# Performance work log

Hardware: AMD Instinct MI355X
Metric: run time of the kernel (lower is better)

The kernel has to match this reference:

```python
import jax, jax.numpy as jnp
import numpy as np


def setup_inputs() -> dict:
    key = jax.random.key(0)
    k1, k2, k3, k4 = jax.random.split(key, 4)
    B, S, D = 8, 2048, 512
    scale = 1.0 / np.sqrt(D)
    return {
        "x": jax.random.normal(k1, (B, S, D), dtype=jnp.float32),
        "WQ": jax.random.normal(k2, (D, D), dtype=jnp.float32) * scale,
        "WK": jax.random.normal(k3, (D, D), dtype=jnp.float32) * scale,
        "WV": jax.random.normal(k4, (D, D), dtype=jnp.float32) * scale,
    }


def reference(x, WQ, WK, WV):
    # x: [B, S, D]; single-head scaled dot-product self-attention
    Q = jnp.einsum("bsd,de->bse", x, WQ)
    K = jnp.einsum("bsd,de->bse", x, WK)
    V = jnp.einsum("bsd,de->bse", x, WV)
    d_k = jnp.asarray(K.shape[-1], dtype=x.dtype)
    scores = jnp.einsum("bqd,bkd->bqk", Q, K) / jnp.sqrt(d_k)  # [B,S,S]
    weights = jax.nn.softmax(scores, axis=-1)
    return jnp.einsum("bqk,bkd->bqd", weights, V)
```

## Files before the change

kernel.cpp:

```cpp
#include <hip/hip_runtime.h>
#include <cstdint>
#include <cstddef>

#define B_ 8
#define S_ 2048
#define D_ 512

typedef float f32x4 __attribute__((ext_vector_type(4)));
typedef __bf16 bf16x8 __attribute__((ext_vector_type(8)));

__device__ __forceinline__ unsigned short f2bf(float f) {
    unsigned u = __builtin_bit_cast(unsigned, f);
    u += 0x7FFFu + ((u >> 16) & 1u);
    return (unsigned short)(u >> 16);
}

__device__ __forceinline__ void gld_lds16(const void* g, void* l) {
    __builtin_amdgcn_global_load_lds(
        (__attribute__((address_space(1))) void*)g,
        (__attribute__((address_space(3))) void*)l,
        16, 0, 0);
}

__global__ __launch_bounds__(256) void gemm_bt(
    const unsigned short* __restrict__ A,
    const unsigned short* __restrict__ B,
    void* __restrict__ Cv,
    int K, int lda, int ldb, int ldc,
    long long sA, long long sB, long long sC,
    float scale, int out_bf16, int ntn, int nbatch)
{
    __shared__ __align__(16) unsigned short lA[128 * 32];
    __shared__ __align__(16) unsigned short lB[128 * 32];

    const int lin = blockIdx.x;
    const int bz  = lin % nbatch;
    const int t   = lin / nbatch;
    const int tn  = t % ntn;
    const int tm  = t / ntn;

    A += (long long)bz * sA;
    B += (long long)bz * sB;
    const int m0 = tm * 128;
    const int n0 = tn * 128;
    const int tid  = threadIdx.x;
    const int lane = tid & 63;
    const int wave = tid >> 6;
    const int wm = (wave & 1) * 64;
    const int wn = (wave >> 1) * 64;

    f32x4 acc[4][4] = {};

    const int bo0 = wave * 2048;
    const int bo1 = bo0 + 1024;
    const int o0 = bo0 + lane * 16;
    const int o1 = bo1 + lane * 16;
    const int r0 = o0 >> 6, cp0 = (o0 & 63) >> 4;
    const int r1 = o1 >> 6, cp1 = (o1 & 63) >> 4;
    const int c0 = (cp0 ^ (r0 & 3)) << 3;
    const int c1 = (cp1 ^ (r1 & 3)) << 3;

    const unsigned short* A0 = A + (size_t)(m0 + r0) * lda + c0;
    const unsigned short* A1 = A + (size_t)(m0 + r1) * lda + c1;
    const unsigned short* B0 = B + (size_t)(n0 + r0) * ldb + c0;
    const unsigned short* B1 = B + (size_t)(n0 + r1) * ldb + c1;

    char* lAc = (char*)lA;
    char* lBc = (char*)lB;

    const int fr  = lane & 15;
    const int g   = lane >> 4;
    const int sx  = (g ^ (fr & 3)) << 3;

    for (int k0 = 0; k0 < K; k0 += 32) {
        __syncthreads();
        gld_lds16(A0 + k0, lAc + bo0);
        gld_lds16(A1 + k0, lAc + bo1);
        gld_lds16(B0 + k0, lBc + bo0);
        gld_lds16(B1 + k0, lBc + bo1);
        __syncthreads();

        bf16x8 af[4], bfr[4];
        #pragma unroll
        for (int tt = 0; tt < 4; ++tt) {
            af[tt]  = *(const bf16x8*)&lA[(wm + tt * 16 + fr) * 32 + sx];
            bfr[tt] = *(const bf16x8*)&lB[(wn + tt * 16 + fr) * 32 + sx];
        }
        #pragma unroll
        for (int mt = 0; mt < 4; ++mt)
            #pragma unroll
            for (int nt = 0; nt < 4; ++nt)
                acc[mt][nt] = __builtin_amdgcn_mfma_f32_16x16x32_bf16(
                    af[mt], bfr[nt], acc[mt][nt], 0, 0, 0);
    }

    const int col = lane & 15;
    const int rb  = (lane >> 4) * 4;
    if (out_bf16) {
        unsigned short* C = (unsigned short*)Cv + (long long)bz * sC;
        #pragma unroll
        for (int mt = 0; mt < 4; ++mt) {
            #pragma unroll
            for (int nt = 0; nt < 4; ++nt) {
                const int gc = n0 + wn + nt * 16 + col;
                #pragma unroll
                for (int r = 0; r < 4; ++r) {
                    const int gr = m0 + wm + mt * 16 + rb + r;
                    C[(size_t)gr * ldc + gc] = f2bf(acc[mt][nt][r] * scale);
                }
            }
        }
    } else {
        float* C = (float*)Cv + (long long)bz * sC;
        #pragma unroll
        for (int mt = 0; mt < 4; ++mt) {
            #pragma unroll
            for (int nt = 0; nt < 4; ++nt) {
                const int gc = n0 + wn + nt * 16 + col;
                #pragma unroll
                for (int r = 0; r < 4; ++r) {
                    const int gr = m0 + wm + mt * 16 + rb + r;
                    C[(size_t)gr * ldc + gc] = acc[mt][nt][r] * scale;
                }
            }
        }
    }
}

__global__ __launch_bounds__(256) void convert_x4(const float* __restrict__ x,
                                                  unsigned short* __restrict__ xb) {
    const size_t i = ((size_t)blockIdx.x * 256 + threadIdx.x) * 4;
    const float4 f = *(const float4*)(x + i);
    ushort4 u;
    u.x = f2bf(f.x); u.y = f2bf(f.y); u.z = f2bf(f.z); u.w = f2bf(f.w);
    *(ushort4*)(xb + i) = u;
}

__global__ __launch_bounds__(256) void convert_w(const float* __restrict__ WQ,
                                                 const float* __restrict__ WK,
                                                 const float* __restrict__ WV,
                                                 unsigned short* __restrict__ WT) {
    const int o = blockIdx.x * 256 + threadIdx.x;
    const float* W = blockIdx.y == 0 ? WQ : (blockIdx.y == 1 ? WK : WV);
    const int e = o >> 9, d = o & (D_ - 1);
    WT[(size_t)blockIdx.y * D_ * D_ + o] = f2bf(W[d * D_ + e]);
}

__global__ __launch_bounds__(256) void transpose_v(const unsigned short* __restrict__ V,
                                                   int ldv,
                                                   unsigned short* __restrict__ VT) {
    __shared__ unsigned short t[32][33];
    const int b  = blockIdx.z;
    const int s0 = blockIdx.x * 32;
    const int d0 = blockIdx.y * 32;
    const int tx = threadIdx.x & 31;
    const int ty = threadIdx.x >> 5;
    const unsigned short* Vb = V + (size_t)b * S_ * ldv;
    unsigned short* VTb = VT + (size_t)b * S_ * D_;
    #pragma unroll
    for (int j = 0; j < 32; j += 8)
        t[ty + j][tx] = Vb[(size_t)(s0 + ty + j) * ldv + d0 + tx];
    __syncthreads();
    #pragma unroll
    for (int j = 0; j < 32; j += 8)
        VTb[(size_t)(d0 + ty + j) * S_ + s0 + tx] = t[tx][ty + j];
}

__global__ __launch_bounds__(256) void softmax_rows(unsigned short* __restrict__ Smat) {
    const int tid = threadIdx.x;
    unsigned short* row = Smat + (size_t)blockIdx.x * S_;
    const uint4 raw = *(const uint4*)(row + tid * 8);
    const unsigned ru[4] = {raw.x, raw.y, raw.z, raw.w};
    float v[8];
    #pragma unroll
    for (int i = 0; i < 4; ++i) {
        v[2 * i]     = __builtin_bit_cast(float, (ru[i] & 0xFFFFu) << 16);
        v[2 * i + 1] = __builtin_bit_cast(float, ru[i] & 0xFFFF0000u);
    }
    float m = v[0];
    #pragma unroll
    for (int i = 1; i < 8; ++i) m = fmaxf(m, v[i]);
    #pragma unroll
    for (int off = 32; off > 0; off >>= 1) m = fmaxf(m, __shfl_xor(m, off, 64));
    __shared__ float red[4];
    const int wave = tid >> 6, lane = tid & 63;
    if (lane == 0) red[wave] = m;
    __syncthreads();
    m = fmaxf(fmaxf(red[0], red[1]), fmaxf(red[2], red[3]));

    float e[8], s = 0.f;
    #pragma unroll
    for (int i = 0; i < 8; ++i) { e[i] = __expf(v[i] - m); s += e[i]; }
    #pragma unroll
    for (int off = 32; off > 0; off >>= 1) s += __shfl_xor(s, off, 64);
    __syncthreads();
    if (lane == 0) red[wave] = s;
    __syncthreads();
    const float inv = 1.0f / (red[0] + red[1] + red[2] + red[3]);

    uint4 o;
    unsigned ov[4];
    #pragma unroll
    for (int i = 0; i < 4; ++i)
        ov[i] = (unsigned)f2bf(e[2 * i] * inv) |
                ((unsigned)f2bf(e[2 * i + 1] * inv) << 16);
    o.x = ov[0]; o.y = ov[1]; o.z = ov[2]; o.w = ov[3];
    *(uint4*)(row + tid * 8) = o;
}

extern "C" void kernel_launch(void* const* d_in, const int* in_sizes, int n_in,
                              void* d_out, int out_size, void* d_ws, size_t ws_size,
                              hipStream_t stream)
{
    const float* x  = (const float*)d_in[0];
    const float* WQ = (const float*)d_in[1];
    const float* WK = (const float*)d_in[2];
    const float* WV = (const float*)d_in[3];

    unsigned short* ws  = (unsigned short*)d_ws;
    const size_t NX = (size_t)B_ * S_ * D_;
    unsigned short* xb  = ws;
    unsigned short* wtb = xb + NX;
    unsigned short* qkv = wtb + 3 * D_ * D_;
    unsigned short* vtb = qkv + NX * 3;
    unsigned short* sb  = vtb + NX;

    convert_x4<<<dim3((unsigned)(NX / 4 / 256)), 256, 0, stream>>>(x, xb);
    convert_w<<<dim3(D_ * D_ / 256, 3), 256, 0, stream>>>(WQ, WK, WV, wtb);

    gemm_bt<<<dim3((B_ * S_ / 128) * (3 * D_ / 128)), 256, 0, stream>>>(
        xb, wtb, qkv, D_, D_, D_, 3 * D_,
        0, 0, 0, 1.0f, 1,  3 * D_ / 128,  1);

    transpose_v<<<dim3(S_ / 32, D_ / 32, B_), 256, 0, stream>>>(
        qkv + 2 * D_, 3 * D_, vtb);

    gemm_bt<<<dim3(B_ * (S_ / 128) * (S_ / 128)), 256, 0, stream>>>(
        qkv , qkv + D_ , sb, D_, 3 * D_, 3 * D_, S_,
        (long long)S_ * 3 * D_, (long long)S_ * 3 * D_, (long long)S_ * S_,
        0.04419417382415922f, 1,  S_ / 128,  B_);

    softmax_rows<<<dim3(B_ * S_), 256, 0, stream>>>(sb);

    gemm_bt<<<dim3(B_ * (S_ / 128) * (D_ / 128)), 256, 0, stream>>>(
        sb, vtb, d_out, S_, S_, S_, D_,
        (long long)S_ * S_, (long long)S_ * D_, (long long)S_ * D_,
        1.0f, 0,  D_ / 128,  B_);
}
```

Baseline: 263.6 us.

## Switch GEMM to 32x32x16 MFMA and fuse V transpose into projection epilogue

Replaces the 16x16x32 MFMA tiling with 32x32x16 bf16 MFMA instructions (2x2 tiles per wave, two k-substeps) and adjusts the LDS swizzle to match. The QKV projection epilogue now writes the V columns directly in transposed [B,D,S] layout, which removes the separate transpose_v kernel and its extra pass over memory. Fewer, larger MFMAs reduce LDS fragment loads per FLOP. The transposed stores are 8-byte strided writes, which may coalesce worse than the row-major stores.

```diff
diff --git a/kernel.cpp b/kernel.cpp
--- a/kernel.cpp
+++ b/kernel.cpp
@@ -6,7 +6,7 @@
 #define S_ 2048
 #define D_ 512
 
-typedef float f32x4 __attribute__((ext_vector_type(4)));
+typedef float f32x16 __attribute__((ext_vector_type(16)));
 typedef __bf16 bf16x8 __attribute__((ext_vector_type(8)));
 
 __device__ __forceinline__ unsigned short f2bf(float f) {
@@ -26,9 +26,10 @@
     const unsigned short* __restrict__ A,
     const unsigned short* __restrict__ B,
     void* __restrict__ Cv,
+    unsigned short* __restrict__ Cv2,
     int K, int lda, int ldb, int ldc,
     long long sA, long long sB, long long sC,
-    float scale, int out_bf16, int ntn, int nbatch)
+    float scale, int mode, int ntn, int nbatch)
 {
     __shared__ __align__(16) unsigned short lA[128 * 32];
     __shared__ __align__(16) unsigned short lB[128 * 32];
@@ -49,7 +50,7 @@
     const int wm = (wave & 1) * 64;
     const int wn = (wave >> 1) * 64;
 
-    f32x4 acc[4][4] = {};
+    f32x16 acc[2][2] = {};
 
     const int bo0 = wave * 2048;
     const int bo1 = bo0 + 1024;
@@ -57,8 +58,8 @@
     const int o1 = bo1 + lane * 16;
     const int r0 = o0 >> 6, cp0 = (o0 & 63) >> 4;
     const int r1 = o1 >> 6, cp1 = (o1 & 63) >> 4;
-    const int c0 = (cp0 ^ (r0 & 3)) << 3;
-    const int c1 = (cp1 ^ (r1 & 3)) << 3;
+    const int c0 = (cp0 ^ ((r0 >> 1) & 3)) << 3;
+    const int c1 = (cp1 ^ ((r1 >> 1) & 3)) << 3;
 
     const unsigned short* A0 = A + (size_t)(m0 + r0) * lda + c0;
     const unsigned short* A1 = A + (size_t)(m0 + r1) * lda + c1;
@@ -68,9 +69,9 @@
     char* lAc = (char*)lA;
     char* lBc = (char*)lB;
 
-    const int fr  = lane & 15;
-    const int g   = lane >> 4;
-    const int sx  = (g ^ (fr & 3)) << 3;
+    const int fr31 = lane & 31;
+    const int g1   = lane >> 5;
+    const int sx0  = ((g1 ^ ((fr31 >> 1) & 3)) << 3);
 
     for (int k0 = 0; k0 < K; k0 += 32) {
         __syncthreads();
@@ -80,47 +81,74 @@
         gld_lds16(B1 + k0, lBc + bo1);
         __syncthreads();
 
-        bf16x8 af[4], bfr[4];
-        #pragma unroll
-        for (int tt = 0; tt < 4; ++tt) {
-            af[tt]  = *(const bf16x8*)&lA[(wm + tt * 16 + fr) * 32 + sx];
-            bfr[tt] = *(const bf16x8*)&lB[(wn + tt * 16 + fr) * 32 + sx];
-        }
-        #pragma unroll
-        for (int mt = 0; mt < 4; ++mt)
-            #pragma unroll
-            for (int nt = 0; nt < 4; ++nt)
-                acc[mt][nt] = __builtin_amdgcn_mfma_f32_16x16x32_bf16(
-                    af[mt], bfr[nt], acc[mt][nt], 0, 0, 0);
+        #pragma unroll
+        for (int ks = 0; ks < 2; ++ks) {
+            const int sx = sx0 ^ (ks << 4);
+            bf16x8 af[2], bfv[2];
+            #pragma unroll
+            for (int mt = 0; mt < 2; ++mt)
+                af[mt] = *(const bf16x8*)&lA[(wm + mt * 32 + fr31) * 32 + sx];
+            #pragma unroll
+            for (int nt = 0; nt < 2; ++nt)
+                bfv[nt] = *(const bf16x8*)&lB[(wn + nt * 32 + fr31) * 32 + sx];
+            #pragma unroll
+            for (int mt = 0; mt < 2; ++mt)
+                #pragma unroll
+                for (int nt = 0; nt < 2; ++nt)
+                    acc[mt][nt] = __builtin_amdgcn_mfma_f32_32x32x16_bf16(
+                        af[mt], bfv[nt], acc[mt][nt], 0, 0, 0);
+        }
     }
 
-    const int col = lane & 15;
-    const int rb  = (lane >> 4) * 4;
-    if (out_bf16) {
-        unsigned short* C = (unsigned short*)Cv + (long long)bz * sC;
-        #pragma unroll
-        for (int mt = 0; mt < 4; ++mt) {
-            #pragma unroll
-            for (int nt = 0; nt < 4; ++nt) {
-                const int gc = n0 + wn + nt * 16 + col;
-                #pragma unroll
-                for (int r = 0; r < 4; ++r) {
-                    const int gr = m0 + wm + mt * 16 + rb + r;
-                    C[(size_t)gr * ldc + gc] = f2bf(acc[mt][nt][r] * scale);
+    const int col = lane & 31;
+
+    if (mode == 2 && tn >= 8) {
+        #pragma unroll
+        for (int mt = 0; mt < 2; ++mt) {
+            #pragma unroll
+            for (int nt = 0; nt < 2; ++nt) {
+                const int d = (n0 - 1024) + wn + nt * 32 + col;
+                #pragma unroll
+                for (int rg = 0; rg < 4; ++rg) {
+                    const int s0q = m0 + wm + mt * 32 + 8 * rg + 4 * g1;
+                    const int b  = s0q >> 11;
+                    const int se = s0q & (S_ - 1);
+                    ushort4 u;
+                    u.x = f2bf(acc[mt][nt][rg * 4 + 0]);
+                    u.y = f2bf(acc[mt][nt][rg * 4 + 1]);
+                    u.z = f2bf(acc[mt][nt][rg * 4 + 2]);
+                    u.w = f2bf(acc[mt][nt][rg * 4 + 3]);
+                    *(ushort4*)&Cv2[((size_t)b * D_ + d) * S_ + se] = u;
                 }
             }
         }
+    } else if (mode >= 1) {
+        unsigned short* C = (unsigned short*)Cv + (long long)bz * sC;
+        #pragma unroll
+        for (int mt = 0; mt < 2; ++mt) {
+            #pragma unroll
+            for (int nt = 0; nt < 2; ++nt) {
+                const int gc = n0 + wn + nt * 32 + col;
+                #pragma unroll
+                for (int reg = 0; reg < 16; ++reg) {
+                    const int gr = m0 + wm + mt * 32 +
+                                   (reg & 3) + 8 * (reg >> 2) + 4 * g1;
+                    C[(size_t)gr * ldc + gc] = f2bf(acc[mt][nt][reg] * scale);
+                }
+            }
+        }
     } else {
         float* C = (float*)Cv + (long long)bz * sC;
         #pragma unroll
-        for (int mt = 0; mt < 4; ++mt) {
-            #pragma unroll
-            for (int nt = 0; nt < 4; ++nt) {
-                const int gc = n0 + wn + nt * 16 + col;
-                #pragma unroll
-                for (int r = 0; r < 4; ++r) {
-                    const int gr = m0 + wm + mt * 16 + rb + r;
-                    C[(size_t)gr * ldc + gc] = acc[mt][nt][r] * scale;
+        for (int mt = 0; mt < 2; ++mt) {
+            #pragma unroll
+            for (int nt = 0; nt < 2; ++nt) {
+                const int gc = n0 + wn + nt * 32 + col;
+                #pragma unroll
+                for (int reg = 0; reg < 16; ++reg) {
+                    const int gr = m0 + wm + mt * 32 +
+                                   (reg & 3) + 8 * (reg >> 2) + 4 * g1;
+                    C[(size_t)gr * ldc + gc] = acc[mt][nt][reg] * scale;
                 }
             }
         }
@@ -146,26 +174,6 @@
     WT[(size_t)blockIdx.y * D_ * D_ + o] = f2bf(W[d * D_ + e]);
 }
 
-__global__ __launch_bounds__(256) void transpose_v(const unsigned short* __restrict__ V,
-                                                   int ldv,
-                                                   unsigned short* __restrict__ VT) {
-    __shared__ unsigned short t[32][33];
-    const int b  = blockIdx.z;
-    const int s0 = blockIdx.x * 32;
-    const int d0 = blockIdx.y * 32;
-    const int tx = threadIdx.x & 31;
-    const int ty = threadIdx.x >> 5;
-    const unsigned short* Vb = V + (size_t)b * S_ * ldv;
-    unsigned short* VTb = VT + (size_t)b * S_ * D_;
-    #pragma unroll
-    for (int j = 0; j < 32; j += 8)
-        t[ty + j][tx] = Vb[(size_t)(s0 + ty + j) * ldv + d0 + tx];
-    __syncthreads();
-    #pragma unroll
-    for (int j = 0; j < 32; j += 8)
-        VTb[(size_t)(d0 + ty + j) * S_ + s0 + tx] = t[tx][ty + j];
-}
-
 __global__ __launch_bounds__(256) void softmax_rows(unsigned short* __restrict__ Smat) {
     const int tid = threadIdx.x;
     unsigned short* row = Smat + (size_t)blockIdx.x * S_;
@@ -221,29 +229,26 @@
     const size_t NX = (size_t)B_ * S_ * D_;
     unsigned short* xb  = ws;
     unsigned short* wtb = xb + NX;
-    unsigned short* qkv = wtb + 3 * D_ * D_;
-    unsigned short* vtb = qkv + NX * 3;
+    unsigned short* qk  = wtb + 3 * D_ * D_;
+    unsigned short* vtb = qk + NX * 2;
     unsigned short* sb  = vtb + NX;
 
     convert_x4<<<dim3((unsigned)(NX / 4 / 256)), 256, 0, stream>>>(x, xb);
     convert_w<<<dim3(D_ * D_ / 256, 3), 256, 0, stream>>>(WQ, WK, WV, wtb);
 
     gemm_bt<<<dim3((B_ * S_ / 128) * (3 * D_ / 128)), 256, 0, stream>>>(
-        xb, wtb, qkv, D_, D_, D_, 3 * D_,
-        0, 0, 0, 1.0f, 1,  3 * D_ / 128,  1);
-
-    transpose_v<<<dim3(S_ / 32, D_ / 32, B_), 256, 0, stream>>>(
-        qkv + 2 * D_, 3 * D_, vtb);
+        xb, wtb, qk, vtb, D_, D_, D_, 2 * D_,
+        0, 0, 0, 1.0f, 2,  3 * D_ / 128,  1);
 
     gemm_bt<<<dim3(B_ * (S_ / 128) * (S_ / 128)), 256, 0, stream>>>(
-        qkv , qkv + D_ , sb, D_, 3 * D_, 3 * D_, S_,
-        (long long)S_ * 3 * D_, (long long)S_ * 3 * D_, (long long)S_ * S_,
+        qk , qk + D_ , sb, nullptr, D_, 2 * D_, 2 * D_, S_,
+        (long long)S_ * 2 * D_, (long long)S_ * 2 * D_, (long long)S_ * S_,
         0.04419417382415922f, 1,  S_ / 128,  B_);
 
     softmax_rows<<<dim3(B_ * S_), 256, 0, stream>>>(sb);
 
     gemm_bt<<<dim3(B_ * (S_ / 128) * (D_ / 128)), 256, 0, stream>>>(
-        sb, vtb, d_out, S_, S_, S_, D_,
-        (long long)S_ * S_, (long long)S_ * D_, (long long)S_ * D_,
+        sb, vtb, d_out, nullptr, S_, S_, S_, D_,
+        (long long)S_ * S_, (long long)D_ * S_, (long long)S_ * D_,
         1.0f, 0,  D_ / 128,  B_);
 }
```

Measured after the change: 258.0 us. 2.1% less time.
